# Optimization experiments

Measured on AMD Instinct MI355X. Metric: run time of the kernel, lower is better.

The kernel has to match this reference:

```python
import jax, jax.numpy as jnp
import numpy as np

ENC_DIM = 64

def setup_inputs() -> dict:
    key = jax.random.key(0)
    ks = jax.random.split(key, 7)
    B, C, H, W = 16, 64, 128, 128
    s = 1.0 / np.sqrt(C)
    return {
        "x": jax.random.normal(ks[0], (B, C, H, W), jnp.float32),
        "wq_w": jax.random.normal(ks[1], (ENC_DIM, C), jnp.float32) * s,
        "wq_b": jax.random.normal(ks[2], (ENC_DIM,), jnp.float32) * 0.01,
        "wk_w": jax.random.normal(ks[3], (ENC_DIM, C), jnp.float32) * s,
        "wk_b": jax.random.normal(ks[4], (ENC_DIM,), jnp.float32) * 0.01,
        "wv_w": jax.random.normal(ks[5], (ENC_DIM, C), jnp.float32) * s,
        "wv_b": jax.random.normal(ks[6], (ENC_DIM,), jnp.float32) * 0.01,
    }

def _conv1x1(x, w, b):
    # 1x1 conv == per-pixel linear: [B,C,H,W] x [E,C] -> [B,E,H,W]
    return jnp.einsum('bchw,ec->behw', x, w) + b[None, :, None, None]

def reference(x, wq_w, wq_b, wk_w, wk_b, wv_w, wv_b):
    scaler = jnp.sqrt(jnp.asarray(ENC_DIM, x.dtype))
    Q = _conv1x1(x, wq_w, wq_b)  # [B,E,H,W]
    K = _conv1x1(x, wk_w, wk_b)
    V = _conv1x1(x, wv_w, wv_b)
    # scores = Q @ K^T over last two dims -> [B,E,H,H]
    scores = jnp.einsum('behw,bekw->behk', Q, K) / scaler
    temp1 = jax.nn.softmax(scores, axis=-1)          # softmax over last dim; dropout is identity (eval)
    # Q^T @ K -> [B,E,W,W], softmax over dim -2
    t2 = jnp.einsum('behw,behv->bewv', Q, K) / scaler
    temp2 = jax.nn.softmax(t2, axis=-2)
    # temp1 @ V @ temp2 -> [B,E,H,W]
    tv = jnp.einsum('behk,bekw->behw', temp1, V)
    return jnp.einsum('behw,bewv->behv', tv, temp2)
```

## Files before the change

kernel.cpp:

```cpp
#include <hip/hip_runtime.h>
#include <hip/hip_bf16.h>

typedef __attribute__((ext_vector_type(8))) short short8;
typedef __attribute__((ext_vector_type(4))) float f32x4;

#define MFMA16(a, b, c) __builtin_amdgcn_mfma_f32_16x16x32_bf16((a), (b), (c), 0, 0, 0)

__device__ __forceinline__ short f2bf(float f) {
  union { float f; unsigned u; } v; v.f = f;
  unsigned r = v.u + 0x7fffu + ((v.u >> 16) & 1u);
  return (short)(r >> 16);
}
__device__ __forceinline__ unsigned pack2(float lo, float hi) {
  return (unsigned)(unsigned short)f2bf(lo) | ((unsigned)(unsigned short)f2bf(hi) << 16);
}

__global__ __launch_bounds__(256) void qkv_kernel(
    const float* __restrict__ x,
    const float* __restrict__ wq, const float* __restrict__ bq,
    const float* __restrict__ wk, const float* __restrict__ bk,
    const float* __restrict__ wv, const float* __restrict__ bv,
    short* __restrict__ Q, short* __restrict__ K, short* __restrict__ V)
{
  __shared__ alignas(16) short xs[64 * 256];
  __shared__ alignas(16) short ws[3 * 64 * 64];
  __shared__ float bs[3 * 64];

  const int t    = threadIdx.x;
  const int b    = blockIdx.x >> 6;
  const int pt   = blockIdx.x & 63;
  const int pix0 = pt << 8;
  const float* xb = x + ((size_t)b << 20);

  #pragma unroll
  for (int i = 0; i < 16; ++i) {
    int f4 = i * 256 + t;
    int c  = f4 >> 6;
    int p4 = (f4 & 63) << 2;
    const float4 v = *reinterpret_cast<const float4*>(xb + c * 16384 + pix0 + p4);
    short* d = &xs[c * 256 + p4];
    d[0] = f2bf(v.x); d[1] = f2bf(v.y); d[2] = f2bf(v.z); d[3] = f2bf(v.w);
  }
  {
    #pragma unroll
    for (int i = 0; i < 16; ++i) {
      int idx = i * 256 + t;
      int e = idx >> 6, c = idx & 63;
      int d = e * 64 + (c ^ ((e & 7) << 3));
      ws[d]        = f2bf(wq[idx]);
      ws[d + 4096] = f2bf(wk[idx]);
      ws[d + 8192] = f2bf(wv[idx]);
    }
    if (t < 192) bs[t] = (t < 64) ? bq[t] : ((t < 128) ? bk[t - 64] : bv[t - 128]);
  }
  __syncthreads();

  const int lane = t & 63;
  const int wid  = t >> 6;
  const int p0   = wid << 6;
  const int l15  = lane & 15;
  const int lg   = lane >> 4;

  short8 bfrag[4][2];
  #pragma unroll
  for (int nt = 0; nt < 4; ++nt) {
    int pix = p0 + nt * 16 + l15;
    #pragma unroll
    for (int ks = 0; ks < 2; ++ks) {
      int cb = ks * 32 + (lg << 3);
      short8 f;
      #pragma unroll
      for (int j = 0; j < 8; ++j) f[j] = xs[(cb + j) * 256 + pix];
      bfrag[nt][ks] = f;
    }
  }

  #pragma unroll
  for (int m = 0; m < 3; ++m) {
    short* op = (m == 0) ? Q : ((m == 1) ? K : V);
    short8 afrag[4][2];
    #pragma unroll
    for (int mt = 0; mt < 4; ++mt) {
      int e = mt * 16 + l15;
      #pragma unroll
      for (int ks = 0; ks < 2; ++ks) {
        int cb8 = (ks * 4 + lg) ^ (e & 7);
        afrag[mt][ks] = *reinterpret_cast<const short8*>(&ws[m * 4096 + e * 64 + cb8 * 8]);
      }
    }
    #pragma unroll
    for (int mt = 0; mt < 4; ++mt) {
      #pragma unroll
      for (int nt = 0; nt < 4; ++nt) {
        f32x4 acc = {0.f, 0.f, 0.f, 0.f};
        acc = MFMA16(afrag[mt][0], bfrag[nt][0], acc);
        acc = MFMA16(afrag[mt][1], bfrag[nt][1], acc);
        int e_base = mt * 16 + (lg << 2);
        int pix = pix0 + p0 + nt * 16 + l15;
        #pragma unroll
        for (int r = 0; r < 4; ++r) {
          int e = e_base + r;
          float val = acc[r] + bs[m * 64 + e];
          op[(((size_t)b * 64 + e) << 14) + pix] = f2bf(val);
        }
      }
    }
  }
}

__global__ __launch_bounds__(512, 4) void attn_kernel(
    const short* __restrict__ Qg, const short* __restrict__ Kg,
    const short* __restrict__ Vg, float* __restrict__ out)
{
  __shared__ alignas(16) short B1[128 * 128];
  __shared__ alignas(16) short B2[128 * 128];

  const int t = threadIdx.x;
  const size_t base = (size_t)blockIdx.x << 14;

  auto stage = [&](short* dst, const short* src) {
    #pragma unroll
    for (int i = 0; i < 4; ++i) {
      int eb  = i * 512 + t;
      int row = eb >> 4;
      int cb  = eb & 15;
      float4 v = *reinterpret_cast<const float4*>(src + (eb << 3));
      *reinterpret_cast<float4*>(dst + row * 128 + ((cb ^ (row & 7)) << 3)) = v;
    }
  };
  auto stageT = [&](short* dst, const short* src) {
    const int w  = t & 127;
    const int rb = (t >> 7) << 5;
    const int w7 = w & 7;
    short v[32];
    #pragma unroll
    for (int k = 0; k < 32; ++k) v[k] = src[(rb + k) * 128 + w];
    #pragma unroll
    for (int k8 = 0; k8 < 4; ++k8) {
      int hb = (rb >> 3) + k8;
      *reinterpret_cast<short8*>(&dst[w * 128 + ((hb ^ w7) << 3)]) =
          *reinterpret_cast<const short8*>(&v[k8 * 8]);
    }
  };

  const int lane = t & 63;
  const int wid  = t >> 6;
  const int m0   = wid << 4;
  const int l15  = lane & 15;
  const int lg   = lane >> 4;

  auto ldfrag = [&](const short* buf, int rowbase, int ks) -> short8 {
    int row = rowbase + l15;
    int cb  = (ks * 4 + lg) ^ (row & 7);
    return *reinterpret_cast<const short8*>(&buf[row * 128 + cb * 8]);
  };

  f32x4 acc[8];

  auto matmul = [&](const short* bufA, const short* bufB) {
    short8 af[4];
    #pragma unroll
    for (int ks = 0; ks < 4; ++ks) af[ks] = ldfrag(bufA, m0, ks);
    #pragma unroll
    for (int n = 0; n < 8; ++n) {
      f32x4 a = {0.f, 0.f, 0.f, 0.f};
      #pragma unroll
      for (int ks = 0; ks < 4; ++ks) a = MFMA16(af[ks], ldfrag(bufB, n * 16, ks), a);
      acc[n] = a;
    }
  };

  auto softmax_pack = [&](unsigned* pk) {
    #pragma unroll
    for (int r = 0; r < 4; ++r) {
      float mx = acc[0][r];
      #pragma unroll
      for (int n = 1; n < 8; ++n) mx = fmaxf(mx, acc[n][r]);
      mx = fmaxf(mx, __shfl_xor(mx, 1));
      mx = fmaxf(mx, __shfl_xor(mx, 2));
      mx = fmaxf(mx, __shfl_xor(mx, 4));
      mx = fmaxf(mx, __shfl_xor(mx, 8));
      float p[8]; float s = 0.f;
      #pragma unroll
      for (int n = 0; n < 8; ++n) { p[n] = __expf((acc[n][r] - mx) * 0.125f); s += p[n]; }
      s += __shfl_xor(s, 1); s += __shfl_xor(s, 2);
      s += __shfl_xor(s, 4); s += __shfl_xor(s, 8);
      float inv = 1.0f / s;
      #pragma unroll
      for (int np = 0; np < 4; ++np)
        pk[r * 4 + np] = pack2(p[2 * np] * inv, p[2 * np + 1] * inv);
    }
  };

  auto store_pk = [&](short* dst, const unsigned* pk) {
    #pragma unroll
    for (int r = 0; r < 4; ++r) {
      int row = m0 + (lg << 2) + r;
      int sw  = (row & 7) << 3;
      #pragma unroll
      for (int np = 0; np < 4; ++np) {
        unsigned v = pk[r * 4 + np];
        int c0 = (2 * np) * 16 + l15;
        int c1 = c0 + 16;
        dst[row * 128 + (c0 ^ sw)] = (short)(v & 0xffff);
        dst[row * 128 + (c1 ^ sw)] = (short)(v >> 16);
      }
    }
  };

  unsigned t1[16], t2[16];

  stage(B1, Qg + base);
  stage(B2, Kg + base);
  __syncthreads();

  matmul(B1, B2);
  softmax_pack(t1);
  __syncthreads();

  stageT(B1, Kg + base);
  stageT(B2, Qg + base);
  __syncthreads();

  matmul(B1, B2);
  softmax_pack(t2);
  __syncthreads();

  store_pk(B1, t1);
  stageT(B2, Vg + base);
  __syncthreads();

  matmul(B1, B2);
  __syncthreads();

  #pragma unroll
  for (int n = 0; n < 8; ++n) {
    #pragma unroll
    for (int r = 0; r < 4; ++r) {
      int row = m0 + (lg << 2) + r;
      int col = n * 16 + l15;
      B1[row * 128 + (col ^ ((row & 7) << 3))] = f2bf(acc[n][r]);
    }
  }
  store_pk(B2, t2);
  __syncthreads();

  float* ob = out + base;
  #pragma unroll
  for (int n = 0; n < 8; ++n) {
    short8 af[4];
    f32x4 a = {0.f, 0.f, 0.f, 0.f};
    #pragma unroll
    for (int ks = 0; ks < 4; ++ks)
      a = MFMA16(ldfrag(B1, m0, ks), ldfrag(B2, n * 16, ks), a);
    (void)af;
    #pragma unroll
    for (int r = 0; r < 4; ++r) {
      int row = m0 + (lg << 2) + r;
      ob[row * 128 + n * 16 + l15] = a[r];
    }
  }
}

extern "C" void kernel_launch(void* const* d_in, const int* in_sizes, int n_in,
                              void* d_out, int out_size, void* d_ws, size_t ws_size,
                              hipStream_t stream) {
  const float* x  = (const float*)d_in[0];
  const float* wq = (const float*)d_in[1];
  const float* bq = (const float*)d_in[2];
  const float* wk = (const float*)d_in[3];
  const float* bk = (const float*)d_in[4];
  const float* wv = (const float*)d_in[5];
  const float* bv = (const float*)d_in[6];

  const size_t N = (size_t)16 * 64 * 128 * 128;
  short* Q = (short*)d_ws;
  short* K = Q + N;
  short* V = K + N;

  qkv_kernel<<<1024, 256, 0, stream>>>(x, wq, bq, wk, bk, wv, bv, Q, K, V);
  attn_kernel<<<1024, 512, 0, stream>>>(Q, K, V, (float*)d_out);
}
```

Before: 97.36 us.

## Build transposed Q/K tiles from LDS instead of re-reading global memory

The transposed Q and K tiles are now built by reading the already staged LDS buffers into registers and writing them back transposed, instead of doing strided 2-byte global loads a second time. The V transposed read is issued early, alongside them, to overlap with compute, and the LDS swizzle is widened from 8 to 16 column groups to reduce bank conflicts. The extra register arrays raise register pressure under the 512x4 launch bounds and could cause spills. One barrier is also moved, which keeps the total barrier count the same.

```diff
diff --git a/kernel.cpp b/kernel.cpp
--- a/kernel.cpp
+++ b/kernel.cpp
@@ -125,21 +125,30 @@
       int row = eb >> 4;
       int cb  = eb & 15;
       float4 v = *reinterpret_cast<const float4*>(src + (eb << 3));
-      *reinterpret_cast<float4*>(dst + row * 128 + ((cb ^ (row & 7)) << 3)) = v;
-    }
-  };
-  auto stageT = [&](short* dst, const short* src) {
-    const int w  = t & 127;
-    const int rb = (t >> 7) << 5;
-    const int w7 = w & 7;
-    short v[32];
-    #pragma unroll
-    for (int k = 0; k < 32; ++k) v[k] = src[(rb + k) * 128 + w];
+      *reinterpret_cast<float4*>(dst + row * 128 + ((cb ^ (row & 15)) << 3)) = v;
+    }
+  };
+
+  const int w  = t & 127;
+  const int rb = (t >> 7) << 5;
+
+  auto t_read = [&](const short* src, unsigned* p) {
+    #pragma unroll
+    for (int k2 = 0; k2 < 16; ++k2) {
+      int r0 = rb + 2 * k2;
+      int r1 = r0 + 1;
+      unsigned a  = (unsigned short)src[r0 * 128 + (w ^ ((r0 & 15) << 3))];
+      unsigned b_ = (unsigned short)src[r1 * 128 + (w ^ ((r1 & 15) << 3))];
+      p[k2] = a | (b_ << 16);
+    }
+  };
+  auto t_write = [&](short* dst, const unsigned* p) {
+    const int w15 = w & 15;
     #pragma unroll
     for (int k8 = 0; k8 < 4; ++k8) {
       int hb = (rb >> 3) + k8;
-      *reinterpret_cast<short8*>(&dst[w * 128 + ((hb ^ w7) << 3)]) =
-          *reinterpret_cast<const short8*>(&v[k8 * 8]);
+      *reinterpret_cast<short8*>(&dst[w * 128 + ((hb ^ w15) << 3)]) =
+          *reinterpret_cast<const short8*>(&p[k8 * 4]);
     }
   };
 
@@ -151,7 +160,7 @@
 
   auto ldfrag = [&](const short* buf, int rowbase, int ks) -> short8 {
     int row = rowbase + l15;
-    int cb  = (ks * 4 + lg) ^ (row & 7);
+    int cb  = (ks * 4 + lg) ^ (row & 15);
     return *reinterpret_cast<const short8*>(&buf[row * 128 + cb * 8]);
   };
 
@@ -196,7 +205,7 @@
     #pragma unroll
     for (int r = 0; r < 4; ++r) {
       int row = m0 + (lg << 2) + r;
-      int sw  = (row & 7) << 3;
+      int sw  = (row & 15) << 3;
       #pragma unroll
       for (int np = 0; np < 4; ++np) {
         unsigned v = pk[r * 4 + np];
@@ -209,6 +218,7 @@
   };
 
   unsigned t1[16], t2[16];
+  unsigned qr[16], kr[16], vr[16];
 
   stage(B1, Qg + base);
   stage(B2, Kg + base);
@@ -216,44 +226,53 @@
 
   matmul(B1, B2);
   softmax_pack(t1);
-  __syncthreads();
-
-  stageT(B1, Kg + base);
-  stageT(B2, Qg + base);
+  t_read(B1, qr);
+  t_read(B2, kr);
+  {
+    const short* Vsrc = Vg + base;
+    #pragma unroll
+    for (int k2 = 0; k2 < 16; ++k2) {
+      unsigned a  = (unsigned short)Vsrc[(rb + 2 * k2) * 128 + w];
+      unsigned b_ = (unsigned short)Vsrc[(rb + 2 * k2 + 1) * 128 + w];
+      vr[k2] = a | (b_ << 16);
+    }
+  }
+  __syncthreads();
+
+  t_write(B1, qr);
+  t_write(B2, kr);
+  __syncthreads();
+
+  matmul(B2, B1);
+  softmax_pack(t2);
+  __syncthreads();
+
+  store_pk(B1, t1);
+  t_write(B2, vr);
   __syncthreads();
 
   matmul(B1, B2);
-  softmax_pack(t2);
-  __syncthreads();
-
-  store_pk(B1, t1);
-  stageT(B2, Vg + base);
-  __syncthreads();
-
-  matmul(B1, B2);
-  __syncthreads();
-
   #pragma unroll
   for (int n = 0; n < 8; ++n) {
     #pragma unroll
     for (int r = 0; r < 4; ++r) {
       int row = m0 + (lg << 2) + r;
       int col = n * 16 + l15;
-      B1[row * 128 + (col ^ ((row & 7) << 3))] = f2bf(acc[n][r]);
-    }
-  }
+      B1[row * 128 + (col ^ ((row & 15) << 3))] = f2bf(acc[n][r]);
+    }
+  }
+  __syncthreads();
+
   store_pk(B2, t2);
   __syncthreads();
 
   float* ob = out + base;
   #pragma unroll
   for (int n = 0; n < 8; ++n) {
-    short8 af[4];
     f32x4 a = {0.f, 0.f, 0.f, 0.f};
     #pragma unroll
     for (int ks = 0; ks < 4; ++ks)
       a = MFMA16(ldfrag(B1, m0, ks), ldfrag(B2, n * 16, ks), a);
-    (void)af;
     #pragma unroll
     for (int r = 0; r < 4; ++r) {
       int row = m0 + (lg << 2) + r;
```

Result: slower. 113.0 us (+16.1%).
